# Kernel tuning notes

Measured on AMD Instinct MI355X. Metric: run time of the kernel, lower is better.

Reference implementation:

```python
import jax, jax.numpy as jnp
import numpy as np

TEMPERATURE = 0.5
EPS = 1e-8  # torch.nn.CosineSimilarity eps


def _l2norm(x):
    # torch cosine sim divides by max(||x||, eps) per vector
    n = jnp.sqrt(jnp.sum(x * x, axis=-1, keepdims=True))
    return x / jnp.maximum(n, EPS)


def setup_inputs() -> dict:
    key = jax.random.key(0)
    ka, kb = jax.random.split(key)
    batch_a = jax.random.normal(ka, (4096, 512), dtype=jnp.float32)
    batch_b = jax.random.normal(kb, (4096, 512), dtype=jnp.float32)
    return {"batch_a": batch_a, "batch_b": batch_b}


def reference(batch_a, batch_b):
    a = _l2norm(batch_a)  # [N, D]
    b = _l2norm(batch_b)
    inv_t = 1.0 / TEMPERATURE
    # cosine similarity via normalize + GEMM (same math as broadcast mul+reduce)
    sim11 = (a @ a.T) * inv_t  # [N, N]
    sim22 = (b @ b.T) * inv_t
    sim12 = (a @ b.T) * inv_t
    n = sim12.shape[-1]
    eye = jnp.eye(n, dtype=bool)
    neg_inf = jnp.float32(-jnp.inf)
    sim11 = jnp.where(eye, neg_inf, sim11)
    sim22 = jnp.where(eye, neg_inf, sim22)
    # logits: [[sim12, sim11], [sim22, sim12^T]] -> [2N, 2N]
    logits = jnp.concatenate(
        [jnp.concatenate([sim12, sim11], axis=-1),
         jnp.concatenate([sim22, sim12.T], axis=-1)],
        axis=-2,
    )
    targets = jnp.arange(2 * n)
    logp = jax.nn.log_softmax(logits, axis=-1)  # stable single pass
    loss = -jnp.mean(logp[jnp.arange(2 * n), targets])
    return loss
```

## Files before the change

kernel.cpp:

```cpp
#include <hip/hip_runtime.h>

#define NR 4096
#define DD 512
#define TWO_N 8192
#define MT 64
#define NTILES 2080
#define CHUNK 260

using bf16x8 = __attribute__((ext_vector_type(8))) short;
using f32x4  = __attribute__((ext_vector_type(4))) float;

__device__ __forceinline__ unsigned short f2bf(float f) {
    union { float f; unsigned u; } v; v.f = f;
    unsigned r = v.u + 0x7fff + ((v.u >> 16) & 1);
    return (unsigned short)(r >> 16);
}

__global__ __launch_bounds__(256) void ntx_nrm_kernel(const float* __restrict__ A,
                                                      const float* __restrict__ B,
                                                      unsigned short* __restrict__ X,
                                                      float* __restrict__ d12,
                                                      float* __restrict__ S) {
    const int row = blockIdx.x;
    const int t = threadIdx.x;
    const int lane = t & 63, wid = t >> 6;

    if (t < 2) S[row * 2 + t] = 0.f;

    const float2 av = *(const float2*)(A + row * DD + 2 * t);
    const float2 bv = *(const float2*)(B + row * DD + 2 * t);
    float sa = av.x * av.x + av.y * av.y;
    float sb = bv.x * bv.x + bv.y * bv.y;
#pragma unroll
    for (int o = 32; o; o >>= 1) { sa += __shfl_down(sa, o); sb += __shfl_down(sb, o); }

    __shared__ float red[12];
    if (lane == 0) { red[wid] = sa; red[4 + wid] = sb; }
    __syncthreads();
    const float ta = red[0] + red[1] + red[2] + red[3];
    const float tb = red[4] + red[5] + red[6] + red[7];
    const float ra = 1.f / fmaxf(sqrtf(ta), 1e-8f);
    const float rb = 1.f / fmaxf(sqrtf(tb), 1e-8f);
    const float nax = av.x * ra, nay = av.y * ra;
    const float nbx = bv.x * rb, nby = bv.y * rb;

    *(unsigned*)(X + row * DD + 2 * t) =
        (unsigned)f2bf(nax) | ((unsigned)f2bf(nay) << 16);
    *(unsigned*)(X + (NR + row) * DD + 2 * t) =
        (unsigned)f2bf(nbx) | ((unsigned)f2bf(nby) << 16);

    float dt = nax * nbx + nay * nby;
#pragma unroll
    for (int o = 32; o; o >>= 1) dt += __shfl_down(dt, o);
    if (lane == 0) red[8 + wid] = dt;
    __syncthreads();
    if (t == 0) d12[row] = red[8] + red[9] + red[10] + red[11];
}

__global__ __launch_bounds__(256) void ntx_gemm_lse_kernel(const unsigned short* __restrict__ X,
                                                           float* __restrict__ S) {
    const int bid = blockIdx.x;
    const int sid = (bid & 7) * CHUNK + (bid >> 3);
    int u, v;
    if (sid < 1792) {
        const int s = sid >> 6, loc = sid & 63;
        int U = 0;
        while (7 * (U + 1) - (U + 1) * U / 2 <= s) ++U;
        const int V = U + 1 + (s - (7 * U - U * (U - 1) / 2));
        u = U * 8 + (loc >> 3);
        v = V * 8 + (loc & 7);
    } else {
        const int s2 = sid - 1792;
        const int U = s2 / 36, loc = s2 % 36;
        int lu = 0;
        while ((lu + 1) * 8 - (lu + 1) * lu / 2 <= loc) ++lu;
        const int lv = lu + (loc - (lu * 8 - lu * (lu - 1) / 2));
        u = U * 8 + lu;
        v = U * 8 + lv;
    }
    const bool fixedTile = (u == v);
    const int rowTile = u * 128, colTile = (v ^ 32) * 128;

    __shared__ unsigned short As[2][128 * 32];
    __shared__ unsigned short Bs[2][128 * 32];

    const int t = threadIdx.x;
    const int lane = t & 63, wid = t >> 6;
    const int waveRow = wid >> 1, waveCol = wid & 1;
    const int lr = lane & 15, grp = lane >> 4;
    const int swr = (lr >> 1) & 3;
    const int kslot = (grp ^ swr) * 8;

    f32x4 acc[4][4] = {};

    const int srow = lane >> 2;
    const int scol = ((lane & 3) ^ ((lane >> 3) & 3)) * 8;

    auto STAGE = [&](int sel, int kt) {
#pragma unroll
        for (int q = 0; q < 2; ++q) {
            const int ci = wid * 2 + q;
            const int r  = ci * 16 + srow;
            const int lo = ci * 512 + lane * 8;
            __builtin_amdgcn_global_load_lds(
                (const __attribute__((address_space(1))) unsigned*)(X + (size_t)(rowTile + r) * DD + kt + scol),
                (__attribute__((address_space(3))) unsigned*)&As[sel][lo], 16, 0, 0);
            __builtin_amdgcn_global_load_lds(
                (const __attribute__((address_space(1))) unsigned*)(X + (size_t)((colTile + r) ^ NR) * DD + kt + scol),
                (__attribute__((address_space(3))) unsigned*)&Bs[sel][lo], 16, 0, 0);
        }
    };

    auto COMPUTE = [&](int sel) {
        bf16x8 af[4], bfr[4];
#pragma unroll
        for (int m = 0; m < 4; ++m)
            af[m] = *(const bf16x8*)&As[sel][(waveRow * 64 + m * 16 + lr) * 32 + kslot];
#pragma unroll
        for (int n = 0; n < 4; ++n)
            bfr[n] = *(const bf16x8*)&Bs[sel][(waveCol * 64 + n * 16 + lr) * 32 + kslot];
        __builtin_amdgcn_s_setprio(1);
#pragma unroll
        for (int m = 0; m < 4; ++m)
#pragma unroll
            for (int n = 0; n < 4; ++n)
                acc[m][n] = __builtin_amdgcn_mfma_f32_16x16x32_bf16(af[m], bfr[n], acc[m][n], 0, 0, 0);
        __builtin_amdgcn_s_setprio(0);
    };

    STAGE(0, 0);
    STAGE(1, 32);
#pragma unroll
    for (int i = 0; i < 16; ++i) {
        const int cur = i & 1;
        if (i < 15) asm volatile("s_waitcnt vmcnt(4)" ::: "memory");
        else        asm volatile("s_waitcnt vmcnt(0)" ::: "memory");
        __builtin_amdgcn_s_barrier();
        COMPUTE(cur);
        if (i < 14) {
            asm volatile("s_waitcnt lgkmcnt(0)" ::: "memory");
            __builtin_amdgcn_s_barrier();
            STAGE(cur, (i + 2) * 32);
        }
    }

#pragma unroll
    for (int m = 0; m < 4; ++m)
#pragma unroll
        for (int n = 0; n < 4; ++n)
#pragma unroll
            for (int reg = 0; reg < 4; ++reg) {
                const int R = rowTile + waveRow * 64 + m * 16 + grp * 4 + reg;
                const int C = colTile + waveCol * 64 + n * 16 + lr;
                const bool masked = fixedTile && (C == (R ^ NR));
                acc[m][n][reg] = masked ? 0.f : __expf(acc[m][n][reg] * 2.0f);
            }

#pragma unroll
    for (int m = 0; m < 4; ++m)
#pragma unroll
        for (int reg = 0; reg < 4; ++reg) {
            float rs = acc[m][0][reg] + acc[m][1][reg] + acc[m][2][reg] + acc[m][3][reg];
            rs += __shfl_xor(rs, 1);
            rs += __shfl_xor(rs, 2);
            rs += __shfl_xor(rs, 4);
            rs += __shfl_xor(rs, 8);
            if (lr == 0) {
                const int R = rowTile + waveRow * 64 + m * 16 + grp * 4 + reg;
                atomicAdd(&S[R], rs);
            }
        }

    if (!fixedTile) {
#pragma unroll
        for (int n = 0; n < 4; ++n) {
            float cs = 0.f;
#pragma unroll
            for (int m = 0; m < 4; ++m)
#pragma unroll
                for (int reg = 0; reg < 4; ++reg)
                    cs += acc[m][n][reg];
            cs += __shfl_xor(cs, 16);
            cs += __shfl_xor(cs, 32);
            if (grp == 0) {
                const int C = colTile + waveCol * 64 + n * 16 + lr;
                atomicAdd(&S[C ^ NR], cs);
            }
        }
    }
}

__global__ __launch_bounds__(256) void ntx_loss_kernel(const float* __restrict__ S,
                                                       const float* __restrict__ d12,
                                                       float* __restrict__ out) {
    const int t = threadIdx.x;
    float a = 0.f;
    for (int r = t; r < TWO_N; r += 256)
        a += __logf(S[r]) - 2.0f * d12[r & (NR - 1)];
    const int lane = t & 63, wid = t >> 6;
#pragma unroll
    for (int o = 32; o; o >>= 1) a += __shfl_down(a, o);
    __shared__ float red[4];
    if (lane == 0) red[wid] = a;
    __syncthreads();
    if (t == 0) out[0] = (red[0] + red[1] + red[2] + red[3]) * (1.f / (float)TWO_N);
}

extern "C" void kernel_launch(void* const* d_in, const int* in_sizes, int n_in,
                              void* d_out, int out_size, void* d_ws, size_t ws_size,
                              hipStream_t stream) {
    const float* A = (const float*)d_in[0];
    const float* B = (const float*)d_in[1];

    unsigned short* X = (unsigned short*)d_ws;
    float* S   = (float*)((char*)d_ws + (size_t)TWO_N * DD * 2);
    float* d12 = (float*)((char*)S + (size_t)TWO_N * 4);

    ntx_nrm_kernel<<<NR, 256, 0, stream>>>(A, B, X, d12, S);

    ntx_gemm_lse_kernel<<<NTILES, 256, 0, stream>>>(X, S);

    ntx_loss_kernel<<<1, 256, 0, stream>>>(S, d12, (float*)d_out);
}
```

Baseline: 90.07 us.

## Enlarge GEMM tiles to 256x256 with 8 waves and 4-stage LDS pipeline

Switches the fused similarity GEMM+exp-sum kernel from 128x128 tiles with 4 waves to 256x256 tiles with 8 waves, each wave computing a 128x64 sub-tile. Staging becomes a 4-buffer ring with loads three k-steps ahead, and the A and B loads are interleaved between two MFMA phases. The aim is more operand reuse per byte loaded, fewer atomics per output, and better hiding of memory latency. In exchange the block count drops to 528, which can leave CUs idle or unevenly loaded, and LDS use and register pressure per block grow.

```diff
diff --git a/kernel.cpp b/kernel.cpp
--- a/kernel.cpp
+++ b/kernel.cpp
@@ -3,9 +3,9 @@
 #define NR 4096
 #define DD 512
 #define TWO_N 8192
-#define MT 64
-#define NTILES 2080
-#define CHUNK 260
+#define MT2 32
+#define NT2 528
+#define CH2 66
 
 using bf16x8 = __attribute__((ext_vector_type(8))) short;
 using f32x4  = __attribute__((ext_vector_type(4))) float;
@@ -57,107 +57,116 @@
     if (t == 0) d12[row] = red[8] + red[9] + red[10] + red[11];
 }
 
-__global__ __launch_bounds__(256) void ntx_gemm_lse_kernel(const unsigned short* __restrict__ X,
-                                                           float* __restrict__ S) {
+__global__ __launch_bounds__(512, 2) void ntx_gemm_lse_kernel(const unsigned short* __restrict__ X,
+                                                              float* __restrict__ S) {
     const int bid = blockIdx.x;
-    const int sid = (bid & 7) * CHUNK + (bid >> 3);
+    const int sid = (bid & 7) * CH2 + (bid >> 3);
     int u, v;
-    if (sid < 1792) {
-        const int s = sid >> 6, loc = sid & 63;
+    if (sid < 448) {
+        const int s = sid >> 4, loc = sid & 15;
         int U = 0;
         while (7 * (U + 1) - (U + 1) * U / 2 <= s) ++U;
         const int V = U + 1 + (s - (7 * U - U * (U - 1) / 2));
-        u = U * 8 + (loc >> 3);
-        v = V * 8 + (loc & 7);
+        u = U * 4 + (loc >> 2);
+        v = V * 4 + (loc & 3);
     } else {
-        const int s2 = sid - 1792;
-        const int U = s2 / 36, loc = s2 % 36;
+        const int s2 = sid - 448;
+        const int U = s2 / 10, loc = s2 % 10;
         int lu = 0;
-        while ((lu + 1) * 8 - (lu + 1) * lu / 2 <= loc) ++lu;
-        const int lv = lu + (loc - (lu * 8 - lu * (lu - 1) / 2));
-        u = U * 8 + lu;
-        v = U * 8 + lv;
+        while ((lu + 1) * 4 - (lu + 1) * lu / 2 <= loc) ++lu;
+        const int lv = lu + (loc - (lu * 4 - lu * (lu - 1) / 2));
+        u = U * 4 + lu;
+        v = U * 4 + lv;
     }
     const bool fixedTile = (u == v);
-    const int rowTile = u * 128, colTile = (v ^ 32) * 128;
-
-    __shared__ unsigned short As[2][128 * 32];
-    __shared__ unsigned short Bs[2][128 * 32];
+    const int rowTile = u * 256, colTile = (v ^ 16) * 256;
+
+    __shared__ unsigned short As[4][256 * 32];
+    __shared__ unsigned short Bs[4][256 * 32];
 
     const int t = threadIdx.x;
     const int lane = t & 63, wid = t >> 6;
-    const int waveRow = wid >> 1, waveCol = wid & 1;
+    const int waveM = wid >> 2, waveN = wid & 3;
     const int lr = lane & 15, grp = lane >> 4;
     const int swr = (lr >> 1) & 3;
     const int kslot = (grp ^ swr) * 8;
 
-    f32x4 acc[4][4] = {};
+    f32x4 acc[8][4] = {};
 
     const int srow = lane >> 2;
     const int scol = ((lane & 3) ^ ((lane >> 3) & 3)) * 8;
 
-    auto STAGE = [&](int sel, int kt) {
+    auto STAGE_A = [&](int sel, int kt) {
 #pragma unroll
         for (int q = 0; q < 2; ++q) {
             const int ci = wid * 2 + q;
             const int r  = ci * 16 + srow;
-            const int lo = ci * 512 + lane * 8;
             __builtin_amdgcn_global_load_lds(
                 (const __attribute__((address_space(1))) unsigned*)(X + (size_t)(rowTile + r) * DD + kt + scol),
-                (__attribute__((address_space(3))) unsigned*)&As[sel][lo], 16, 0, 0);
+                (__attribute__((address_space(3))) unsigned*)&As[sel][ci * 512 + lane * 8], 16, 0, 0);
+        }
+    };
+    auto STAGE_B = [&](int sel, int kt) {
+#pragma unroll
+        for (int q = 0; q < 2; ++q) {
+            const int ci = wid * 2 + q;
+            const int r  = ci * 16 + srow;
             __builtin_amdgcn_global_load_lds(
                 (const __attribute__((address_space(1))) unsigned*)(X + (size_t)((colTile + r) ^ NR) * DD + kt + scol),
-                (__attribute__((address_space(3))) unsigned*)&Bs[sel][lo], 16, 0, 0);
+                (__attribute__((address_space(3))) unsigned*)&Bs[sel][ci * 512 + lane * 8], 16, 0, 0);
         }
     };
 
-    auto COMPUTE = [&](int sel) {
-        bf16x8 af[4], bfr[4];
-#pragma unroll
-        for (int m = 0; m < 4; ++m)
-            af[m] = *(const bf16x8*)&As[sel][(waveRow * 64 + m * 16 + lr) * 32 + kslot];
-#pragma unroll
-        for (int n = 0; n < 4; ++n)
-            bfr[n] = *(const bf16x8*)&Bs[sel][(waveCol * 64 + n * 16 + lr) * 32 + kslot];
+    auto PHASE = [&](int sel, int mbase, bf16x8* bfr) {
+        bf16x8 af[4];
+#pragma unroll
+        for (int mm = 0; mm < 4; ++mm)
+            af[mm] = *(const bf16x8*)&As[sel][(waveM * 128 + (mbase + mm) * 16 + lr) * 32 + kslot];
         __builtin_amdgcn_s_setprio(1);
 #pragma unroll
-        for (int m = 0; m < 4; ++m)
+        for (int mm = 0; mm < 4; ++mm)
 #pragma unroll
             for (int n = 0; n < 4; ++n)
-                acc[m][n] = __builtin_amdgcn_mfma_f32_16x16x32_bf16(af[m], bfr[n], acc[m][n], 0, 0, 0);
+                acc[mbase + mm][n] = __builtin_amdgcn_mfma_f32_16x16x32_bf16(af[mm], bfr[n], acc[mbase + mm][n], 0, 0, 0);
         __builtin_amdgcn_s_setprio(0);
     };
 
-    STAGE(0, 0);
-    STAGE(1, 32);
-#pragma unroll
-    for (int i = 0; i < 16; ++i) {
-        const int cur = i & 1;
-        if (i < 15) asm volatile("s_waitcnt vmcnt(4)" ::: "memory");
-        else        asm volatile("s_waitcnt vmcnt(0)" ::: "memory");
+    STAGE_A(0, 0);   STAGE_B(0, 0);
+    STAGE_A(1, 32);  STAGE_B(1, 32);
+    STAGE_A(2, 64);  STAGE_B(2, 64);
+
+#pragma unroll
+    for (int tt = 0; tt < 16; ++tt) {
+        const int sel = tt & 3;
+        asm volatile("s_waitcnt lgkmcnt(0)" ::: "memory");
+        if (tt <= 13)      asm volatile("s_waitcnt vmcnt(8)" ::: "memory");
+        else if (tt == 14) asm volatile("s_waitcnt vmcnt(4)" ::: "memory");
+        else               asm volatile("s_waitcnt vmcnt(0)" ::: "memory");
         __builtin_amdgcn_s_barrier();
-        COMPUTE(cur);
-        if (i < 14) {
-            asm volatile("s_waitcnt lgkmcnt(0)" ::: "memory");
-            __builtin_amdgcn_s_barrier();
-            STAGE(cur, (i + 2) * 32);
-        }
+        bf16x8 bfr[4];
+#pragma unroll
+        for (int n = 0; n < 4; ++n)
+            bfr[n] = *(const bf16x8*)&Bs[sel][(waveN * 64 + n * 16 + lr) * 32 + kslot];
+        if (tt < 13) STAGE_A((tt + 3) & 3, (tt + 3) * 32);
+        PHASE(sel, 0, bfr);
+        if (tt < 13) STAGE_B((tt + 3) & 3, (tt + 3) * 32);
+        PHASE(sel, 4, bfr);
     }
 
 #pragma unroll
-    for (int m = 0; m < 4; ++m)
+    for (int m = 0; m < 8; ++m)
 #pragma unroll
         for (int n = 0; n < 4; ++n)
 #pragma unroll
             for (int reg = 0; reg < 4; ++reg) {
-                const int R = rowTile + waveRow * 64 + m * 16 + grp * 4 + reg;
-                const int C = colTile + waveCol * 64 + n * 16 + lr;
+                const int R = rowTile + waveM * 128 + m * 16 + grp * 4 + reg;
+                const int C = colTile + waveN * 64 + n * 16 + lr;
                 const bool masked = fixedTile && (C == (R ^ NR));
                 acc[m][n][reg] = masked ? 0.f : __expf(acc[m][n][reg] * 2.0f);
             }
 
 #pragma unroll
-    for (int m = 0; m < 4; ++m)
+    for (int m = 0; m < 8; ++m)
 #pragma unroll
         for (int reg = 0; reg < 4; ++reg) {
             float rs = acc[m][0][reg] + acc[m][1][reg] + acc[m][2][reg] + acc[m][3][reg];
@@ -166,7 +175,7 @@
             rs += __shfl_xor(rs, 4);
             rs += __shfl_xor(rs, 8);
             if (lr == 0) {
-                const int R = rowTile + waveRow * 64 + m * 16 + grp * 4 + reg;
+                const int R = rowTile + waveM * 128 + m * 16 + grp * 4 + reg;
                 atomicAdd(&S[R], rs);
             }
         }
@@ -176,14 +185,14 @@
         for (int n = 0; n < 4; ++n) {
             float cs = 0.f;
 #pragma unroll
-            for (int m = 0; m < 4; ++m)
+            for (int m = 0; m < 8; ++m)
 #pragma unroll
                 for (int reg = 0; reg < 4; ++reg)
                     cs += acc[m][n][reg];
             cs += __shfl_xor(cs, 16);
             cs += __shfl_xor(cs, 32);
             if (grp == 0) {
-                const int C = colTile + waveCol * 64 + n * 16 + lr;
+                const int C = colTile + waveN * 64 + n * 16 + lr;
                 atomicAdd(&S[C ^ NR], cs);
             }
         }
@@ -218,7 +227,7 @@
 
     ntx_nrm_kernel<<<NR, 256, 0, stream>>>(A, B, X, d12, S);
 
-    ntx_gemm_lse_kernel<<<NTILES, 256, 0, stream>>>(X, S);
+    ntx_gemm_lse_kernel<<<NT2, 512, 0, stream>>>(X, S);
 
     ntx_loss_kernel<<<1, 256, 0, stream>>>(S, d12, (float*)d_out);
 }
```

Result: no change. 90.15 us (+0.1%).
